# Kernel tuning notes

Measured on AMD Instinct MI355X. Metric: run time of the kernel, lower is better.

## Reference

```python
import jax, jax.numpy as jnp
import numpy as np

TOP_K_PERCENT = 0.25  # top_k_percent_pixels from init_kwargs
B, C, H, W = 8, 19, 512, 1024


def setup_inputs() -> dict:
    key = jax.random.key(0)
    k1, k2 = jax.random.split(key)
    logits = jax.random.normal(k1, (B, C, H, W), dtype=jnp.float32)
    labels = jax.random.randint(k2, (B, H, W), 0, C)  # int labels, in-range
    return {"logits": logits, "labels": labels}


def reference(logits, labels):
    # loss_fn: per-pixel cross-entropy with reduction='none' -> [B, H, W]
    logZ = jax.nn.logsumexp(logits, axis=1)  # [B, H, W], stable softmax normalizer
    gathered = jnp.take_along_axis(logits, labels[:, None, :, :], axis=1)[:, 0]  # [B, H, W]
    loss = logZ - gathered  # per-pixel CE
    # get_topk_percent: flatten non-batch dims, keep top k = pct * num_pixels per row
    flat = loss.reshape(loss.shape[0], -1)  # [B, H*W]
    num_pixels = flat.shape[1]
    k = int(TOP_K_PERCENT * num_pixels)
    top_vals, _ = jax.lax.top_k(flat, k)  # [B, k]
    return top_vals.mean()
```

## Files before the change

### kernel.cpp

```cpp
#include <hip/hip_runtime.h>
#include <cstdint>

#define BB   8
#define CC   19
#define HWP  524288
#define NPIX 4194304
#define KSEL 131072
#define GRID 4096

#define H1_OFF   0
#define H2_OFF   (8*2048)
#define H3_OFF   (H2_OFF + 8*4096)
#define SEL1_OFF (H3_OFF + 8*256)
#define CNT1_OFF (SEL1_OFF + 8)
#define SEL2_OFF (CNT1_OFF + 8)
#define CNT2_OFF (SEL2_OFF + 8)
#define PAD_OFF  (CNT2_OFF + 8)
#define SUMA_OFF (PAD_OFF + 2)
#define CTRL_WORDS (SUMA_OFF + 16)
#define LOSS_BYTES (NPIX * 4)


__device__ __forceinline__ uint32_t block_incl_scan_u32(uint32_t v, volatile uint32_t* wt) {
    int lane = threadIdx.x & 63, wid = threadIdx.x >> 6;
    uint32_t inc = v;
#pragma unroll
    for (int off = 1; off < 64; off <<= 1) {
        uint32_t t = __shfl_up(inc, off);
        if (lane >= off) inc += t;
    }
    __syncthreads();
    if (lane == 63) wt[wid] = inc;
    __syncthreads();
    for (int w = 0; w < wid; w++) inc += wt[w];
    return inc;
}

__device__ __forceinline__ double block_reduce_double(double v, volatile double* dwt) {
    int lane = threadIdx.x & 63, wid = threadIdx.x >> 6;
#pragma unroll
    for (int off = 32; off > 0; off >>= 1) v += __shfl_down(v, off);
    __syncthreads();
    if (lane == 0) dwt[wid] = v;
    __syncthreads();
    return dwt[0] + dwt[1] + dwt[2] + dwt[3];
}

__device__ __forceinline__ void block_sum_atomic(double sum, double* dst, volatile double* dwt) {
    double t = block_reduce_double(sum, dwt);
    if (threadIdx.x == 0 && t != 0.0) atomicAdd(dst, t);
}

template <int NBINS>
__device__ __forceinline__ void row_select(
    const uint32_t* __restrict__ hrow, uint32_t prev,
    volatile uint32_t* wt, volatile uint32_t* shSel, volatile uint32_t* shCnt,
    uint32_t& sel, uint32_t& cnt)
{
    constexpr int CH = NBINS / 256;
    int base = NBINS - CH * ((int)threadIdx.x + 1);
    uint32_t hloc[CH];
    uint32_t csum = 0;
#pragma unroll
    for (int i = 0; i < CH; i++) { hloc[i] = hrow[base + i]; csum += hloc[i]; }
    uint32_t incl = block_incl_scan_u32(csum, wt);
    uint32_t pre = incl - csum;
    uint32_t target = (uint32_t)KSEL - prev;
    if (pre < target && pre + csum >= target) {
        uint32_t cum = pre;
#pragma unroll
        for (int i = CH - 1; i >= 0; i--) {
            uint32_t h = hloc[i];
            if (cum + h >= target) { *shSel = (uint32_t)(base + i); *shCnt = prev + cum; break; }
            cum += h;
        }
    }
    __syncthreads();
    sel = *shSel; cnt = *shCnt;
}


__global__ __launch_bounds__(256) void loss_hist1(
    const float* __restrict__ logits, const int* __restrict__ labels,
    float* __restrict__ loss, uint32_t* __restrict__ hist1)
{
    __shared__ uint32_t lh[2048];
    for (int i = threadIdx.x; i < 2048; i += 256) lh[i] = 0u;
    __syncthreads();

    int b = blockIdx.x >> 9;
    int pix0 = blockIdx.x * 1024 + threadIdx.x * 4;
    int prow = pix0 & (HWP - 1);

    const float4* lg = (const float4*)(logits + (size_t)b * CC * HWP + prow);
    float4 a[CC];
#pragma unroll
    for (int c = 0; c < CC; c++) a[c] = lg[(size_t)c * (HWP / 4)];

    int4 lab = *(const int4*)(labels + pix0);

    float mx0 = a[0].x, mx1 = a[0].y, mx2 = a[0].z, mx3 = a[0].w;
#pragma unroll
    for (int c = 1; c < CC; c++) {
        mx0 = fmaxf(mx0, a[c].x); mx1 = fmaxf(mx1, a[c].y);
        mx2 = fmaxf(mx2, a[c].z); mx3 = fmaxf(mx3, a[c].w);
    }
    float g0 = 0.f, g1 = 0.f, g2 = 0.f, g3 = 0.f;
    float e0 = 0.f, e1 = 0.f, e2 = 0.f, e3 = 0.f;
#pragma unroll
    for (int c = 0; c < CC; c++) {
        e0 += __expf(a[c].x - mx0); e1 += __expf(a[c].y - mx1);
        e2 += __expf(a[c].z - mx2); e3 += __expf(a[c].w - mx3);
        g0 = (lab.x == c) ? a[c].x : g0;
        g1 = (lab.y == c) ? a[c].y : g1;
        g2 = (lab.z == c) ? a[c].z : g2;
        g3 = (lab.w == c) ? a[c].w : g3;
    }
    float l0 = fmaxf(mx0 + __logf(e0) - g0, 0.f);
    float l1 = fmaxf(mx1 + __logf(e1) - g1, 0.f);
    float l2 = fmaxf(mx2 + __logf(e2) - g2, 0.f);
    float l3 = fmaxf(mx3 + __logf(e3) - g3, 0.f);

    float4 o; o.x = l0; o.y = l1; o.z = l2; o.w = l3;
    *(float4*)(loss + pix0) = o;

    atomicAdd(&lh[__float_as_uint(l0) >> 20], 1u);
    atomicAdd(&lh[__float_as_uint(l1) >> 20], 1u);
    atomicAdd(&lh[__float_as_uint(l2) >> 20], 1u);
    atomicAdd(&lh[__float_as_uint(l3) >> 20], 1u);

    __syncthreads();
    for (int i = threadIdx.x; i < 2048; i += 256) {
        uint32_t v = lh[i];
        if (v) atomicAdd(&hist1[b * 2048 + i], v);
    }
}


__global__ __launch_bounds__(256) void refine2s(
    const float* __restrict__ loss, const uint32_t* __restrict__ hist1,
    uint32_t* __restrict__ hist2,
    uint32_t* __restrict__ sel1g, uint32_t* __restrict__ cnt1g,
    double* __restrict__ sumAbove)
{
    __shared__ uint32_t lh[4096];
    __shared__ uint32_t wt[4];
    __shared__ double dwt[4];
    __shared__ uint32_t shSel, shCnt;
    for (int i = threadIdx.x; i < 4096; i += 256) lh[i] = 0u;
    __syncthreads();

    int b = blockIdx.x >> 9;
    int rowblk = blockIdx.x & 511;

    uint32_t s1, c1;
    row_select<2048>(hist1 + b * 2048, 0u, wt, &shSel, &shCnt, s1, c1);
    if (rowblk == 0 && threadIdx.x == 0) { sel1g[b] = s1; cnt1g[b] = c1; }
    __syncthreads();

    int pix0 = blockIdx.x * 1024 + threadIdx.x * 4;
    float4 v = *(const float4*)(loss + pix0);

    double sum = 0.0;
    {
        float vv[4] = {v.x, v.y, v.z, v.w};
#pragma unroll
        for (int j = 0; j < 4; j++) {
            uint32_t u = __float_as_uint(vv[j]);
            uint32_t t = u >> 20;
            if (t > s1) sum += (double)vv[j];
            else if (t == s1) atomicAdd(&lh[(u >> 8) & 0xFFFu], 1u);
        }
    }
    __syncthreads();
    block_sum_atomic(sum, &sumAbove[b], dwt);
    for (int i = threadIdx.x; i < 4096; i += 256) {
        uint32_t c = lh[i];
        if (c) atomicAdd(&hist2[b * 4096 + i], c);
    }
}


__global__ __launch_bounds__(256) void refine3s(
    const float* __restrict__ loss, const uint32_t* __restrict__ hist2,
    uint32_t* __restrict__ hist3,
    const uint32_t* __restrict__ sel1g, const uint32_t* __restrict__ cnt1g,
    uint32_t* __restrict__ sel2g, uint32_t* __restrict__ cnt2g,
    double* __restrict__ sumAbove)
{
    __shared__ uint32_t lh[256];
    __shared__ uint32_t wt[4];
    __shared__ double dwt[4];
    __shared__ uint32_t shSel, shCnt;
    lh[threadIdx.x] = 0u;
    __syncthreads();

    int b = blockIdx.x >> 9;
    int rowblk = blockIdx.x & 511;
    uint32_t s1 = sel1g[b];
    uint32_t c1 = cnt1g[b];

    uint32_t s2, c2;
    row_select<4096>(hist2 + b * 4096, c1, wt, &shSel, &shCnt, s2, c2);
    if (rowblk == 0 && threadIdx.x == 0) { sel2g[b] = s2; cnt2g[b] = c2; }
    __syncthreads();

    int pix0 = blockIdx.x * 1024 + threadIdx.x * 4;
    float4 v = *(const float4*)(loss + pix0);

    double sum = 0.0;
    {
        float vv[4] = {v.x, v.y, v.z, v.w};
#pragma unroll
        for (int j = 0; j < 4; j++) {
            uint32_t u = __float_as_uint(vv[j]);
            if ((u >> 20) == s1) {
                uint32_t mid = (u >> 8) & 0xFFFu;
                if (mid > s2) sum += (double)vv[j];
                else if (mid == s2) atomicAdd(&lh[u & 0xFFu], 1u);
            }
        }
    }
    __syncthreads();
    block_sum_atomic(sum, &sumAbove[b], dwt);
    {
        uint32_t c = lh[threadIdx.x];
        if (c) atomicAdd(&hist3[b * 256 + threadIdx.x], c);
    }
}


__global__ __launch_bounds__(256) void finalize_k(
    const uint32_t* __restrict__ hist3,
    const uint32_t* __restrict__ sel1, const uint32_t* __restrict__ sel2,
    const uint32_t* __restrict__ cnt2, const double* __restrict__ sumAbove,
    float* __restrict__ out)
{
    __shared__ uint32_t wt[4];
    __shared__ double dwt[4];
    double tot = 0.0;
    for (int r = 0; r < BB; r++) {
        int b3 = 255 - (int)threadIdx.x;
        uint32_t h = hist3[r * 256 + b3];
        uint32_t incl = block_incl_scan_u32(h, wt);
        uint32_t pre = incl - h;
        uint32_t rem = (uint32_t)KSEL - cnt2[r];
        uint32_t take = (rem > pre) ? ((rem - pre < h) ? (rem - pre) : h) : 0u;
        uint32_t P = (sel1[r] << 20) | (sel2[r] << 8) | (uint32_t)b3;
        double contrib = (double)take * (double)__uint_as_float(P);
        double s = block_reduce_double(contrib, dwt);
        if (threadIdx.x == 0) tot += s + sumAbove[r];
    }
    if (threadIdx.x == 0) out[0] = (float)(tot / ((double)BB * (double)KSEL));
}

extern "C" void kernel_launch(void* const* d_in, const int* in_sizes, int n_in,
                              void* d_out, int out_size, void* d_ws, size_t ws_size,
                              hipStream_t stream)
{
    const float* logits = (const float*)d_in[0];
    const int* labels   = (const int*)d_in[1];
    float* out          = (float*)d_out;

    char* ws = (char*)d_ws;
    float* loss      = (float*)ws;
    uint32_t* ctrl   = (uint32_t*)(ws + LOSS_BYTES);
    uint32_t* hist1  = ctrl + H1_OFF;
    uint32_t* hist2  = ctrl + H2_OFF;
    uint32_t* hist3  = ctrl + H3_OFF;
    uint32_t* sel1   = ctrl + SEL1_OFF;
    uint32_t* cnt1   = ctrl + CNT1_OFF;
    uint32_t* sel2   = ctrl + SEL2_OFF;
    uint32_t* cnt2   = ctrl + CNT2_OFF;
    double* sumAbove = (double*)(ctrl + SUMA_OFF);

    (void)hipMemsetAsync(ctrl, 0, CTRL_WORDS * sizeof(uint32_t), stream);
    loss_hist1<<<GRID, 256, 0, stream>>>(logits, labels, loss, hist1);
    refine2s<<<GRID, 256, 0, stream>>>(loss, hist1, hist2, sel1, cnt1, sumAbove);
    refine3s<<<GRID, 256, 0, stream>>>(loss, hist2, hist3, sel1, cnt1, sel2, cnt2, sumAbove);
    finalize_k<<<1, 256, 0, stream>>>(hist3, sel1, sel2, cnt2, sumAbove, out);
}
```

Before: 541.6 us.

## Fuse refine passes and finalize into one cooperative kernel with register-held loss

Replaces the refine2s, refine3s and finalize launches with a single cooperative-groups kernel that loads each block's loss values into registers once. It reuses them for both refinement passes, separated by grid-wide syncs, so the loss buffer is read once instead of twice and two launches go away. The kernel needs 2048 or 1024 blocks co-resident. It tries the wider grid first when the occupancy query allows and falls back to the old three-kernel path otherwise. Grid syncs and the single-block finalize add serialization cost.

Result: no change. 544.5 us (+0.5%).

```diff
diff --git a/kernel.cpp b/kernel.cpp
--- a/kernel.cpp
+++ b/kernel.cpp
@@ -1,5 +1,8 @@
 #include <hip/hip_runtime.h>
+#include <hip/hip_cooperative_groups.h>
 #include <cstdint>
+
+namespace cg = cooperative_groups;
 
 #define BB   8
 #define CC   19
@@ -137,6 +140,105 @@
 }
 
 
+template <int RBLK, int NG>
+__global__ __launch_bounds__(256) void refine_coop(
+    const float* __restrict__ loss,
+    const uint32_t* __restrict__ hist1, uint32_t* __restrict__ hist2,
+    uint32_t* __restrict__ hist3,
+    uint32_t* __restrict__ sel1g, uint32_t* __restrict__ sel2g,
+    uint32_t* __restrict__ cnt2g, double* __restrict__ sumAbove,
+    float* __restrict__ out)
+{
+    cg::grid_group grid = cg::this_grid();
+    __shared__ uint32_t lh[4096];
+    __shared__ uint32_t wt[4];
+    __shared__ double dwt[4];
+    __shared__ uint32_t shSel, shCnt;
+
+    const int tid = threadIdx.x;
+    const int b = (int)blockIdx.x / RBLK;
+    const int rowblk = (int)blockIdx.x % RBLK;
+
+    for (int i = tid; i < 4096; i += 256) lh[i] = 0u;
+
+    float4 lr[NG];
+    const int pbase = b * HWP + rowblk * (1024 * NG) + tid * 4;
+#pragma unroll
+    for (int g = 0; g < NG; g++)
+        lr[g] = *(const float4*)(loss + pbase + g * 1024);
+
+    uint32_t s1, c1;
+    row_select<2048>(hist1 + b * 2048, 0u, wt, &shSel, &shCnt, s1, c1);
+    if (rowblk == 0 && tid == 0) sel1g[b] = s1;
+
+    double sum = 0.0;
+#pragma unroll
+    for (int g = 0; g < NG; g++) {
+        float vv[4] = {lr[g].x, lr[g].y, lr[g].z, lr[g].w};
+#pragma unroll
+        for (int j = 0; j < 4; j++) {
+            uint32_t u = __float_as_uint(vv[j]);
+            uint32_t t = u >> 20;
+            if (t > s1) sum += (double)vv[j];
+            else if (t == s1) atomicAdd(&lh[(u >> 8) & 0xFFFu], 1u);
+        }
+    }
+    __syncthreads();
+    block_sum_atomic(sum, &sumAbove[b], dwt);
+    for (int i = tid; i < 4096; i += 256) {
+        uint32_t c = lh[i];
+        if (c) atomicAdd(&hist2[b * 4096 + i], c);
+    }
+    grid.sync();
+
+    uint32_t s2, c2;
+    row_select<4096>(hist2 + b * 4096, c1, wt, &shSel, &shCnt, s2, c2);
+    if (rowblk == 0 && tid == 0) { sel2g[b] = s2; cnt2g[b] = c2; }
+    __syncthreads();
+    lh[tid] = 0u;
+    __syncthreads();
+
+    double sum2 = 0.0;
+#pragma unroll
+    for (int g = 0; g < NG; g++) {
+        float vv[4] = {lr[g].x, lr[g].y, lr[g].z, lr[g].w};
+#pragma unroll
+        for (int j = 0; j < 4; j++) {
+            uint32_t u = __float_as_uint(vv[j]);
+            if ((u >> 20) == s1) {
+                uint32_t mid = (u >> 8) & 0xFFFu;
+                if (mid > s2) sum2 += (double)vv[j];
+                else if (mid == s2) atomicAdd(&lh[u & 0xFFu], 1u);
+            }
+        }
+    }
+    __syncthreads();
+    block_sum_atomic(sum2, &sumAbove[b], dwt);
+    {
+        uint32_t c = lh[tid];
+        if (c) atomicAdd(&hist3[b * 256 + tid], c);
+    }
+    grid.sync();
+
+    if (blockIdx.x == 0) {
+        double tot = 0.0;
+        for (int r = 0; r < BB; r++) {
+            int b3 = 255 - tid;
+            uint32_t h = hist3[r * 256 + b3];
+            uint32_t incl = block_incl_scan_u32(h, wt);
+            uint32_t pre = incl - h;
+            uint32_t rem = (uint32_t)KSEL - cnt2g[r];
+            uint32_t take = (rem > pre) ? ((rem - pre < h) ? (rem - pre) : h) : 0u;
+            uint32_t P = (sel1g[r] << 20) | (sel2g[r] << 8) | (uint32_t)b3;
+            double contrib = (double)take * (double)__uint_as_float(P);
+            double s = block_reduce_double(contrib, dwt);
+            if (tid == 0) tot += s + sumAbove[r];
+        }
+        if (tid == 0) out[0] = (float)(tot / ((double)BB * (double)KSEL));
+    }
+}
+
+
 __global__ __launch_bounds__(256) void refine2s(
     const float* __restrict__ loss, const uint32_t* __restrict__ hist1,
     uint32_t* __restrict__ hist2,
@@ -179,7 +281,6 @@
         if (c) atomicAdd(&hist2[b * 4096 + i], c);
     }
 }
-
 
 __global__ __launch_bounds__(256) void refine3s(
     const float* __restrict__ loss, const uint32_t* __restrict__ hist2,
@@ -228,7 +329,6 @@
         if (c) atomicAdd(&hist3[b * 256 + threadIdx.x], c);
     }
 }
-
 
 __global__ __launch_bounds__(256) void finalize_k(
     const uint32_t* __restrict__ hist3,
@@ -276,6 +376,38 @@
 
     (void)hipMemsetAsync(ctrl, 0, CTRL_WORDS * sizeof(uint32_t), stream);
     loss_hist1<<<GRID, 256, 0, stream>>>(logits, labels, loss, hist1);
+
+    {
+        const float* a0 = loss;
+        const uint32_t* a1 = hist1;
+        uint32_t* a2 = hist2;
+        uint32_t* a3 = hist3;
+        uint32_t* a4 = sel1;
+        uint32_t* a5 = sel2;
+        uint32_t* a6 = cnt2;
+        double*   a7 = sumAbove;
+        float*    a8 = out;
+        void* args[9] = { (void*)&a0, (void*)&a1, (void*)&a2, (void*)&a3,
+                          (void*)&a4, (void*)&a5, (void*)&a6, (void*)&a7, (void*)&a8 };
+
+        int nb = 0;
+        if (hipOccupancyMaxActiveBlocksPerMultiprocessor(&nb, refine_coop<256, 2>, 256, 0) == hipSuccess
+            && nb >= 8) {
+            if (hipLaunchCooperativeKernel(refine_coop<256, 2>, dim3(256 * BB), dim3(256),
+                                           args, 0, stream) == hipSuccess)
+                return;
+            (void)hipGetLastError();
+        }
+        nb = 0;
+        if (hipOccupancyMaxActiveBlocksPerMultiprocessor(&nb, refine_coop<128, 4>, 256, 0) == hipSuccess
+            && nb >= 4) {
+            if (hipLaunchCooperativeKernel(refine_coop<128, 4>, dim3(128 * BB), dim3(256),
+                                           args, 0, stream) == hipSuccess)
+                return;
+            (void)hipGetLastError();
+        }
+    }
+
     refine2s<<<GRID, 256, 0, stream>>>(loss, hist1, hist2, sel1, cnt1, sumAbove);
     refine3s<<<GRID, 256, 0, stream>>>(loss, hist2, hist3, sel1, cnt1, sel2, cnt2, sumAbove);
     finalize_k<<<1, 256, 0, stream>>>(hist3, sel1, sel2, cnt2, sumAbove, out);
```
